# Kernel tuning notes

Measured on AMD Instinct MI355X. Metric: run time of the kernel, lower is better.

## Reference

```python
import jax, jax.numpy as jnp
import numpy as np

N_CLUSTERS = 10

def _conv(x, w, b, stride):
    y = jax.lax.conv_general_dilated(x, w, stride, 'VALID', dimension_numbers=('NCHW', 'OIHW', 'NCHW'))
    return y + b[None, :, None, None]

def _forward(x, conv1_w, conv1_b, conv2_w, conv2_b, conv3_w, conv3_b,
             anc0_w, anc0_b, anc1_w, anc1_b, anc2_w, anc2_b, anc3_w, anc3_b,
             W1_w, W1_b, U_w, U_b, V_w, V_b, Wa_w, Wa_b,
             cluster_w, cluster_b, cls_w, cls_b):
    # backbone: three stride-2 valid convs
    h1 = _conv(x, conv1_w, conv1_b, (2, 2))
    h2 = _conv(h1, conv2_w, conv2_b, (2, 2))
    h3 = _conv(h2, conv3_w, conv3_b, (2, 2))  # [1,512,63,63]
    ancs = [_conv(h3, anc0_w, anc0_b, (1, 1)),
            _conv(h3, anc1_w, anc1_b, (1, 1)),
            _conv(h3, anc2_w, anc2_b, (1, 1)),
            _conv(h3, anc3_w, anc3_b, (1, 1))]
    ksizes = [(3, 3), (1, 1), (3, 1), (1, 3)]
    Hf, Wf = h3.shape[2], h3.shape[3]
    feats, coords = [], []
    # feat_organizer: flatten each anchor map to [Ha*Wa, 1024] and build normalized box coords
    for a, (kh, kw) in zip(ancs, ksizes):
        C, Ha, Wa = a.shape[1], a.shape[2], a.shape[3]
        feats.append(a[0].reshape(C, Ha * Wa).T)
        ys, xs = jnp.meshgrid(jnp.arange(Ha, dtype=jnp.float32), jnp.arange(Wa, dtype=jnp.float32), indexing='ij')
        cx = (xs.reshape(-1) + kw * 0.5) / Wf
        cy = (ys.reshape(-1) + kh * 0.5) / Hf
        bw = jnp.full((Ha * Wa,), kw / Wf, jnp.float32)
        bh = jnp.full((Ha * Wa,), kh / Hf, jnp.float32)
        coords.append(jnp.stack([cx, cy, bw, bh], axis=1))
    feat = jnp.concatenate(feats, 0)      # [N,1024]
    coords = jnp.concatenate(coords, 0)   # [N,4]
    # gated-attention MLP (AttentionHead)
    hmid = jax.nn.relu(feat @ W1_w.T + W1_b)              # [N,512]
    u = jax.nn.sigmoid(hmid @ U_w.T + U_b)                # [N,256]
    v = jnp.tanh(hmid @ V_w.T + V_b)                      # [N,256]
    att = jax.nn.sigmoid((u * v) @ Wa_w.T + Wa_b)[:, 0]   # [N]
    # cluster_features: rank anchors by attention, split into equal clusters,
    # attention-weighted segment reduce of features and box coords per cluster
    N = att.shape[0]
    rank = jnp.argsort(jnp.argsort(-att))
    cid = (rank * N_CLUSTERS) // N                         # [N] int cluster ids
    sw = jax.ops.segment_sum(att, cid, num_segments=N_CLUSTERS)                       # [nc]
    fc = jax.ops.segment_sum(hmid * att[:, None], cid, num_segments=N_CLUSTERS) / (sw[:, None] + 1e-8)   # [nc,512]
    pc = jax.ops.segment_sum(coords * att[:, None], cid, num_segments=N_CLUSTERS) / (sw[:, None] + 1e-8) # [nc,4]
    # ClusterAttention: conv with kernel (1,512) == per-cluster dot product, softmax over clusters
    scores = fc @ cluster_w + cluster_b                    # [nc]
    att_c = jax.nn.softmax(scores)
    # attention_pooling: attention-weighted sum of cluster features
    final = (att_c[:, None] * fc).sum(0, keepdims=True)    # [1,512]
    logits = final @ cls_w.T + cls_b
    return jax.nn.softmax(logits, axis=1), att_c.reshape(1, N_CLUSTERS, 1), pc

def setup_inputs() -> dict:
    key = jax.random.key(0)
    ks = jax.random.split(key, 30)
    def rn(k, shape, scale=0.02):
        return jax.random.normal(k, shape, jnp.float32) * scale
    d = {}
    d['x'] = jax.random.normal(ks[0], (1, 3, 512, 512), jnp.float32)
    d['conv1_w'] = rn(ks[1], (128, 3, 3, 3));    d['conv1_b'] = jnp.zeros((128,), jnp.float32)
    d['conv2_w'] = rn(ks[2], (256, 128, 3, 3));  d['conv2_b'] = jnp.zeros((256,), jnp.float32)
    d['conv3_w'] = rn(ks[3], (512, 256, 3, 3));  d['conv3_b'] = jnp.zeros((512,), jnp.float32)
    d['anc0_w'] = rn(ks[4], (1024, 512, 3, 3));  d['anc0_b'] = jnp.zeros((1024,), jnp.float32)
    d['anc1_w'] = rn(ks[5], (1024, 512, 1, 1));  d['anc1_b'] = jnp.zeros((1024,), jnp.float32)
    d['anc2_w'] = rn(ks[6], (1024, 512, 3, 1));  d['anc2_b'] = jnp.zeros((1024,), jnp.float32)
    d['anc3_w'] = rn(ks[7], (1024, 512, 1, 3));  d['anc3_b'] = jnp.zeros((1024,), jnp.float32)
    d['W1_w'] = rn(ks[8], (512, 1024));          d['W1_b'] = jnp.zeros((512,), jnp.float32)
    d['U_w'] = rn(ks[9], (256, 512));            d['U_b'] = jnp.zeros((256,), jnp.float32)
    d['V_w'] = rn(ks[10], (256, 512));           d['V_b'] = jnp.zeros((256,), jnp.float32)
    d['Wa_w'] = rn(ks[11], (1, 256));            d['Wa_b'] = jnp.zeros((1,), jnp.float32)
    d['cluster_w'] = rn(ks[12], (512,));         d['cluster_b'] = jnp.zeros((), jnp.float32)
    d['cls_w'] = rn(ks[13], (10, 512));          d['cls_b'] = jnp.zeros((10,), jnp.float32)
    return d

def reference(x, conv1_w, conv1_b, conv2_w, conv2_b, conv3_w, conv3_b,
              anc0_w, anc0_b, anc1_w, anc1_b, anc2_w, anc2_b, anc3_w, anc3_b,
              W1_w, W1_b, U_w, U_b, V_w, V_b, Wa_w, Wa_b,
              cluster_w, cluster_b, cls_w, cls_b):
    return _forward(x, conv1_w, conv1_b, conv2_w, conv2_b, conv3_w, conv3_b,
                    anc0_w, anc0_b, anc1_w, anc1_b, anc2_w, anc2_b, anc3_w, anc3_b,
                    W1_w, W1_b, U_w, U_b, V_w, V_b, Wa_w, Wa_b,
                    cluster_w, cluster_b, cls_w, cls_b)
```

## Files before the change

### kernel.cpp

```cpp
#include <hip/hip_runtime.h>
#include <math.h>


#define NTOT 15376
#define PHALF 2032128
typedef unsigned short u16;
typedef unsigned long long u64;
typedef __attribute__((ext_vector_type(8))) short bf16x8;
typedef __attribute__((ext_vector_type(4))) float f32x4;

static __device__ __forceinline__ u16 f2bf(float x) {
    union { float f; unsigned u; } v; v.f = x;
    unsigned r = v.u + 0x7FFF + ((v.u >> 16) & 1);
    return (u16)(r >> 16);
}
static __device__ __forceinline__ float bf2f(u16 h) {
    union { unsigned u; float f; } v; v.u = ((unsigned)h) << 16;
    return v.f;
}

static __device__ __forceinline__ void glds16(const void* g, void* l) {
    __builtin_amdgcn_global_load_lds(
        (const __attribute__((address_space(1))) void*)g,
        (__attribute__((address_space(3))) void*)l,
        16, 0, 0);
}

__global__ __launch_bounds__(256) void prep_all(
    const float* __restrict__ s4, const float* __restrict__ s5,
    const float* __restrict__ s6, const float* __restrict__ s7,
    const float* __restrict__ s8, u16* __restrict__ Wpk,
    u16* __restrict__ UVsep,
    const float* __restrict__ c1w, u16* __restrict__ Wc1pk,
    const float* __restrict__ x, u16* __restrict__ x_t,
    const float* __restrict__ W1w, const float* __restrict__ W1b,
    const float* __restrict__ b0, const float* __restrict__ b1,
    const float* __restrict__ b2, const float* __restrict__ b3,
    float* __restrict__ hb)
{
    int b = blockIdx.x, t = threadIdx.x;
    if (b < 8832) {
        long i = (long)b * 256 + t;
        if (i >= 2260992L) return;
        if (i < 524288L) {
            Wpk[8388608L + i] = f2bf(s4[i]);
        } else if (i < 786432L) {
            long loc = i - 524288L;
            int ic = (int)(loc % 512);
            long row = loc / 512;
            const float* src = (row & 1) ? s6 : s5;
            UVsep[loc] = f2bf(src[(row >> 1) * 512 + ic]);
        } else if (i < 1081344L) {
            long loc = i - 786432L;
            int ic = (int)(loc % 128);
            long r = loc / 128;
            int tt = (int)(r % 9);
            long oc = r / 9;
            Wpk[9175040L + loc] = f2bf(s7[(oc * 128 + ic) * 9 + tt]);
        } else {
            long loc = i - 1081344L;
            int ic = (int)(loc % 256);
            long r = loc / 256;
            int tt = (int)(r % 9);
            long oc = r / 9;
            Wpk[9469952L + loc] = f2bf(s8[(oc * 256 + ic) * 9 + tt]);
        }
    } else if (b < 8864) {
        int j = (b - 8832) * 256 + t;
        if (j < 8192) {
            int oc = j >> 6, k = j & 63;
            Wc1pk[j] = (k < 27) ? f2bf(c1w[oc * 27 + k]) : (u16)0;
        }
    } else if (b < 9119) {
        int sp = (b - 8864) * 256 + t;
        if (sp < 65025) {
            int oy = sp / 255, ox = sp - oy * 255;
            const float* base = x + (long)oy * 2 * 512 + ox * 2;
            u64 pk[16];
#pragma unroll
            for (int q = 0; q < 16; ++q) pk[q] = 0;
#pragma unroll
            for (int ic = 0; ic < 3; ++ic)
#pragma unroll
                for (int ky = 0; ky < 3; ++ky)
#pragma unroll
                    for (int kx = 0; kx < 3; ++kx) {
                        int k = ic * 9 + ky * 3 + kx;
                        float v = base[ic * 262144 + ky * 512 + kx];
                        pk[k >> 2] |= (u64)f2bf(v) << ((k & 3) * 16);
                    }
            u64* drow = (u64*)(x_t + (long)sp * 64);
#pragma unroll
            for (int q = 0; q < 16; ++q) drow[q] = pk[q];
        }
    } else {
        int w = t >> 6, l = t & 63;
        int idx = (b - 9119) * 4 + w;
        int a = idx >> 9, m = idx & 511;
        const float* ab = (a == 0) ? b0 : (a == 1) ? b1 : (a == 2) ? b2 : b3;
        float s = 0.f;
        for (int j = l; j < 1024; j += 64)
            s = fmaf(W1w[(long)m * 1024 + j], ab[j], s);
#pragma unroll
        for (int d = 1; d < 64; d <<= 1) s += __shfl_xor(s, d, 64);
        if (l == 0) hb[idx] = s + W1b[m];
    }
}

__global__ __launch_bounds__(256) void packT_anchor(
    const float* __restrict__ a0w, const float* __restrict__ a1w,
    const float* __restrict__ a2w, const float* __restrict__ a3w,
    u16* __restrict__ WpkT)
{
    __shared__ u16 tile[64][65];
    int bid = blockIdx.x;
    int ocb = bid & 15;
    int rt  = bid >> 4;
    const float* src; int kbase, NT;
    if      (rt < 72)  { src = a0w; kbase = 0;    NT = 9; }
    else if (rt < 80)  { src = a1w; kbase = 4608; NT = 1; }
    else if (rt < 104) { src = a2w; kbase = 5120; NT = 3; }
    else               { src = a3w; kbase = 6656; NT = 3; }
    int kloc0 = rt * 64 - kbase;
    int tap = kloc0 >> 9, ic0 = kloc0 & 511;
    int t = threadIdx.x, q = t >> 6, ln = t & 63;
#pragma unroll
    for (int i = 0; i < 16; ++i) {
        int ocl = q * 16 + i;
        tile[ocl][ln] = f2bf(src[((long)(ocb * 64 + ocl) * 512 + ic0 + ln) * NT + tap]);
    }
    __syncthreads();
#pragma unroll
    for (int i = 0; i < 16; ++i) {
        int kl = q * 16 + i;
        WpkT[(long)(rt * 64 + kl) * 1024 + ocb * 64 + ln] = tile[ln][kl];
    }
}

__global__ __launch_bounds__(256) void combA(
    const float* __restrict__ P, const float* __restrict__ hb,
    u16* __restrict__ Hfeat)
{
    int row = blockIdx.x;
    int oy = row / 61, ox = row - oy * 61;
    long n = (long)(oy * 63 + ox) * 512;
    int c = threadIdx.x * 2;
    float2 p0 = *(const float2*)(P + n + c);
    float2 p1 = *(const float2*)(P + PHALF + n + c);
    float2 bv = *(const float2*)(hb + c);
    float sx = (p0.x + p1.x) + bv.x;
    float sy = (p0.y + p1.y) + bv.y;
    unsigned pk = (unsigned)f2bf(fmaxf(sx, 0.f))
                | ((unsigned)f2bf(fmaxf(sy, 0.f)) << 16);
    *(unsigned*)(Hfeat + (long)row * 512 + c) = pk;
}

__global__ __launch_bounds__(256) void comb3(
    const float* __restrict__ P, const float* __restrict__ bias,
    u16* __restrict__ h3T)
{
    int row = blockIdx.x;
    int trg = (row / 63) * 65 + row % 63;
    long n = (long)row * 512;
    int c = threadIdx.x * 2;
    float2 q0 = *(const float2*)(P + n + c);
    float2 q1 = *(const float2*)(P + PHALF + n + c);
    float2 b  = *(const float2*)(bias + c);
    unsigned pk = (unsigned)f2bf(q0.x + q1.x + b.x)
                | ((unsigned)f2bf(q0.y + q1.y + b.y) << 16);
    *(unsigned*)(h3T + (long)trg * 512 + c) = pk;
}

template<int CMODE, int EMODE, int TMODE>
__global__ __launch_bounds__(256) void gemm_bt(
    const u16* __restrict__ A, const u16* __restrict__ B,
    const float* __restrict__ bias0, const float* __restrict__ bias1,
    const float* __restrict__ bias2, const float* __restrict__ bias3,
    void* __restrict__ Cout, float* __restrict__ Pbuf,
    int M, int N, int RSB, int Ktot, int OH, int OW, int obase)
{
    __shared__ u16 As[4096];
    __shared__ u16 Bs[8192];
    const int tid = threadIdx.x, w = tid >> 6, l = tid & 63;
    const int wr = w >> 1, wc = w & 1;
    const int sl = l & 7, sh = l >> 3, sx = sl ^ sh;

    int n0, m0;
    bool TW3 = false;
    int part = -1;
    int tbase = 0;
    const float* bias = bias0;
    constexpr int ICL2 = (TMODE == 5) ? 1 : (TMODE == 6) ? 2 : (TMODE == 9) ? 0 : 3;
    constexpr int ICK  = 1 << ICL2;
    int ntaps;

    if (TMODE == 8) {
        int job = blockIdx.x >> 8, sub = blockIdx.x & 255;
        n0 = (sub & 31) * 128; m0 = (sub >> 5) * 64;
        int anc;
        if      (job == 0) { anc = 0; ntaps = 4; tbase = 0; part = 0; }
        else if (job == 1) { anc = 0; ntaps = 5; tbase = 4; part = 1; }
        else if (job == 2) { anc = 1; ntaps = 1; }
        else if (job == 3) { anc = 2; ntaps = 3; }
        else               { anc = 3; ntaps = 3; }
        TW3 = (anc == 0 || anc == 3);
        A += (anc == 0) ? 0 : (anc == 1) ? 4608 : (anc == 2) ? 5120 : 6656;
        obase = (anc == 0) ? 0 : (anc == 1) ? 3721 : (anc == 2) ? 7690 : 11533;
        OH = (anc == 0 || anc == 2) ? 61 : 63;
        OW = (anc == 0 || anc == 3) ? 61 : 63;
        bias = bias0 + anc * 512;
    } else if (TMODE == 6 && EMODE == 7) {
        int half = blockIdx.y >> 3;
        n0 = blockIdx.x * 128; m0 = (blockIdx.y & 7) * 64;
        ntaps = half ? 5 : 4; tbase = half * 4;
        Cout = (void*)((float*)Cout + (long)half * PHALF);
    } else {
        n0 = blockIdx.x * 128; m0 = blockIdx.y * 64;
        ntaps = Ktot >> ICL2;
    }
    const long RSA = (TMODE == 8) ? 8192 : (long)Ktot * 64;
    const long RSB2 = (long)RSB * 2;

    int offB[4], ldsOffB[4], ldsOffA[2];
    const char* aBase[2];
    const char* bBase[4];
#pragma unroll
    for (int j = 0; j < 4; ++j) {
        int r = w * 32 + j * 8 + sh;
        int gn = n0 + r;
        if (CMODE == 0)      { gn = min(gn, 3968);  offB[j] = (gn / 63) * 65 + (gn % 63); }
        else if (CMODE == 1) { offB[j] = min(gn, N - 1); }
        else if (CMODE == 2) { gn = min(gn, 16128); offB[j] = (gn / 127) * 510 + (gn % 127) * 2; }
        else                 { gn = min(gn, 3968);  offB[j] = (gn / 63) * 254 + (gn % 63) * 2; }
        ldsOffB[j] = r * 128;
        bBase[j] = (const char*)B + (long)offB[j] * RSB2 + sx * 16;
    }
#pragma unroll
    for (int j = 0; j < 2; ++j) {
        int r = w * 16 + j * 8 + sh;
        ldsOffA[j] = r * 128;
        aBase[j] = (const char*)A + (long)(m0 + r) * RSA * 2 + sx * 16;
    }

    f32x4 acc[2][4];
#pragma unroll
    for (int a = 0; a < 2; ++a)
#pragma unroll
        for (int b = 0; b < 4; ++b) acc[a][b] = (f32x4){0.f, 0.f, 0.f, 0.f};

    for (int t_ = 0; t_ < ntaps; ++t_) {
        int te = t_ + tbase;
        long tOffB;
        if (TMODE == 8) {
            int trow_;
            if (TW3) { int q_ = (te * 11) >> 5; trow_ = q_ * 65 + (te - q_ * 3); }
            else       trow_ = te * 65;
            tOffB = (long)trow_ * RSB2;
        } else if (TMODE == 4) {
            tOffB = (long)te * 1024;
        } else if (TMODE == 5) {
            int q_ = (te * 11) >> 5;
            tOffB = (long)(q_ * 255 + (te - q_ * 3)) * RSB2;
        } else if (TMODE == 6) {
            int q_ = (te * 11) >> 5;
            tOffB = (long)(q_ * 127 + (te - q_ * 3)) * RSB2;
        } else {
            tOffB = 0;
        }
        long aOff = (long)te * (ICK * 128);
#pragma unroll
        for (int kb = 0; kb < ICK; ++kb) {
#pragma unroll
            for (int j = 0; j < 2; ++j)
                glds16(aBase[j] + aOff + kb * 128, (char*)As + ldsOffA[j]);
#pragma unroll
            for (int j = 0; j < 4; ++j)
                glds16(bBase[j] + tOffB + kb * 128, (char*)Bs + ldsOffB[j]);
            __syncthreads();
#pragma unroll
            for (int kk = 0; kk < 2; ++kk) {
                bf16x8 af[2], bfr[4];
#pragma unroll
                for (int f = 0; f < 2; ++f) {
                    int rm = wr * 32 + f * 16 + (l & 15);
                    af[f] = *(const bf16x8*)((const char*)As + rm * 128 +
                               (((kk * 4 + (l >> 4)) ^ (rm & 7)) * 16));
                }
#pragma unroll
                for (int f = 0; f < 4; ++f) {
                    int rn = wc * 64 + f * 16 + (l & 15);
                    bfr[f] = *(const bf16x8*)((const char*)Bs + rn * 128 +
                               (((kk * 4 + (l >> 4)) ^ (rn & 7)) * 16));
                }
#pragma unroll
                for (int fm = 0; fm < 2; ++fm)
#pragma unroll
                    for (int fn = 0; fn < 4; ++fn)
                        acc[fm][fn] = __builtin_amdgcn_mfma_f32_16x16x32_bf16(
                            af[fm], bfr[fn], acc[fm][fn], 0, 0, 0);
            }
            __syncthreads();
        }
    }

#pragma unroll
    for (int fm = 0; fm < 2; ++fm) {
        int gmb = m0 + wr * 32 + fm * 16 + (l >> 4) * 4;
#pragma unroll
        for (int fn = 0; fn < 4; ++fn) {
            int gn = n0 + wc * 64 + fn * 16 + (l & 15);
            f32x4 v = acc[fm][fn];
            if (EMODE == 2) {
                if (gn < N) {
                    int j0 = gmb >> 1;
                    float u0 = 1.f / (1.f + expf(-(v.x + bias0[j0])));
                    float t0 = tanhf(v.y + bias1[j0]);
                    float u1 = 1.f / (1.f + expf(-(v.z + bias0[j0 + 1])));
                    float t1 = tanhf(v.w + bias1[j0 + 1]);
                    float2 o = { u0 * t0 * bias2[j0], u1 * t1 * bias2[j0 + 1] };
                    *(float2*)((float*)Cout + (long)gn * 256 + j0) = o;
                }
            } else if (EMODE == 4) {
                if (gn < N) {
                    float4 bv = *(const float4*)(bias + gmb);
                    u64 pk = (u64)f2bf(v.x + bv.x)
                           | ((u64)f2bf(v.y + bv.y) << 16)
                           | ((u64)f2bf(v.z + bv.z) << 32)
                           | ((u64)f2bf(v.w + bv.w) << 48);
                    *(u64*)((u16*)Cout + (long)gn * M + gmb) = pk;
                }
            } else if (EMODE == 5) {
                if (TMODE == 8 && part >= 0) {
                    if (gn < 3969) {
                        float4 o = { v.x, v.y, v.z, v.w };
                        *(float4*)(Pbuf + (long)part * PHALF + (long)gn * 512 + gmb) = o;
                    }
                } else if (gn < 3969) {
                    int oy = gn / 63, ox = gn - oy * 63;
                    if (oy < OH && ox < OW) {
                        int trg = obase + oy * OW + ox;
                        float4 bv = *(const float4*)(bias + gmb);
                        u64 pk = (u64)f2bf(fmaxf(v.x + bv.x, 0.f))
                               | ((u64)f2bf(fmaxf(v.y + bv.y, 0.f)) << 16)
                               | ((u64)f2bf(fmaxf(v.z + bv.z, 0.f)) << 32)
                               | ((u64)f2bf(fmaxf(v.w + bv.w, 0.f)) << 48);
                        *(u64*)((u16*)Cout + (long)trg * M + gmb) = pk;
                    }
                }
            } else if (EMODE == 6) {
                if (gn < N) {
                    u64 pk = (u64)f2bf(v.x)
                           | ((u64)f2bf(v.y) << 16)
                           | ((u64)f2bf(v.z) << 32)
                           | ((u64)f2bf(v.w) << 48);
                    *(u64*)((u16*)Cout + (long)gn * M + gmb) = pk;
                }
            } else {
                if (gn < 3969) {
                    float4 o = { v.x, v.y, v.z, v.w };
                    *(float4*)((float*)Cout + (long)gn * 512 + gmb) = o;
                }
            }
        }
    }
}

__global__ __launch_bounds__(256) void att_v3(
    const float* __restrict__ UVw, const float* __restrict__ Wab,
    float* __restrict__ att, int* __restrict__ rank, int N)
{
    int t = threadIdx.x, l = t & 63, r = t >> 6;
    int n = blockIdx.x * 4 + r;
    if (t < 4 && blockIdx.x * 4 + t < N) rank[blockIdx.x * 4 + t] = 0;
    if (n >= N) return;
    float4 p = *(const float4*)(UVw + (long)n * 256 + l * 4);
    float s = (p.x + p.y) + (p.z + p.w);
#pragma unroll
    for (int d = 1; d < 64; d <<= 1) s += __shfl_xor(s, d, 64);
    if (l == 0) att[n] = 1.f / (1.f + expf(-(s + Wab[0])));
}

__global__ __launch_bounds__(256) void rank_partial(
    const float* __restrict__ att, int* __restrict__ rank, int N)
{
    __shared__ float sa[1024];
    int n = blockIdx.x * 256 + threadIdx.x;
    int base = blockIdx.y * 1024;
    int cnt = min(1024, N - base);
    for (int t = threadIdx.x; t < cnt; t += 256) sa[t] = att[base + t];
    __syncthreads();
    if (n >= N) return;
    float a = att[n];
    int r = 0;
    for (int t = 0; t < cnt; ++t) {
        float aj = sa[t];
        int j = base + t;
        r += (int)(aj > a) | ((int)(aj == a) & (int)(j < n));
    }
    atomicAdd(&rank[n], r);
}

#define FC_NB 256
#define FC_ROWS 61
__device__ __forceinline__ void anchor_coords(int n, float& cx, float& cy,
                                              float& bw, float& bh)
{
    int kh, kw, Wa, loc;
    if (n < 3721)       { kh = 3; kw = 3; Wa = 61; loc = n; }
    else if (n < 7690)  { kh = 1; kw = 1; Wa = 63; loc = n - 3721; }
    else if (n < 11533) { kh = 3; kw = 1; Wa = 63; loc = n - 7690; }
    else                { kh = 1; kw = 3; Wa = 61; loc = n - 11533; }
    int iy = loc / Wa, ix = loc - iy * Wa;
    cx = (ix + kw * 0.5f) * (1.f / 63.f);
    cy = (iy + kh * 0.5f) * (1.f / 63.f);
    bw = kw * (1.f / 63.f);
    bh = kh * (1.f / 63.f);
}

__global__ __launch_bounds__(256) void tail_part(
    const u16* __restrict__ Hfeat, const float* __restrict__ att,
    const int* __restrict__ rank, float* __restrict__ fcp,
    float* __restrict__ prt, int N)
{
    __shared__ float red[4][50];
    int t = threadIdx.x;
    if (blockIdx.x < FC_NB) {
        int b = blockIdx.x;
        int l = t & 63, r = t >> 6;
        float acc[10][8];
#pragma unroll
        for (int k = 0; k < 10; ++k)
#pragma unroll
            for (int e = 0; e < 8; ++e) acc[k][e] = 0.f;
        int n0 = b * FC_ROWS;
        for (int it = 0; it < 16; ++it) {
            int nl = it * 4 + r;
            int n = n0 + nl;
            if (nl >= FC_ROWS || n >= N) break;
            float a = att[n];
            int c = (rank[n] * 10) / N;
            bf16x8 h8 = *(const bf16x8*)(Hfeat + (long)n * 512 + l * 8);
            float hf[8];
#pragma unroll
            for (int e = 0; e < 8; ++e) hf[e] = bf2f((u16)h8[e]);
#pragma unroll
            for (int k = 0; k < 10; ++k) {
                float sel = (c == k) ? a : 0.f;
#pragma unroll
                for (int e = 0; e < 8; ++e)
                    acc[k][e] = fmaf(sel, hf[e], acc[k][e]);
            }
        }
        float* dst = fcp + (long)b * 5120 + l * 8;
#pragma unroll
        for (int k = 0; k < 10; ++k)
#pragma unroll
            for (int e = 0; e < 8; ++e) dst[k * 512 + e] = acc[k][e];
    } else {
        int b = blockIdx.x - FC_NB;
        int n = b * 256 + t;
        int l = t & 63, w = t >> 6;
        float a = 0.f, cx = 0.f, cy = 0.f, bw = 0.f, bh = 0.f;
        int c = -1;
        if (n < N) {
            a = att[n]; c = (rank[n] * 10) / N;
            anchor_coords(n, cx, cy, bw, bh);
        }
#pragma unroll
        for (int k = 0; k < 10; ++k) {
            float sel = (c == k) ? a : 0.f;
            float v[5] = {sel, sel * cx, sel * cy, sel * bw, sel * bh};
#pragma unroll
            for (int d = 0; d < 5; ++d) {
                float x = v[d];
#pragma unroll
                for (int s = 1; s < 64; s <<= 1) x += __shfl_xor(x, s, 64);
                if (l == 0) red[w][k * 5 + d] = x;
            }
        }
        __syncthreads();
        if (t < 50) prt[b * 50 + t] = red[0][t] + red[1][t] + red[2][t] + red[3][t];
    }
}

__global__ __launch_bounds__(256) void fc_sum(
    const float* __restrict__ fcp, float* __restrict__ fc_raw)
{
    int i = blockIdx.x * 256 + threadIdx.x;
    if (i >= 5120) return;
    float s = 0.f;
    for (int b = 0; b < FC_NB; ++b) s += fcp[(long)b * 5120 + i];
    fc_raw[i] = s;
}

__global__ __launch_bounds__(512) void final_kernel(
    const float* __restrict__ fc_raw, const float* __restrict__ prt,
    const float* __restrict__ cluster_w, const float* __restrict__ cluster_b,
    const float* __restrict__ cls_w, const float* __restrict__ cls_b,
    float* __restrict__ out)
{
    __shared__ float red[512];
    __shared__ float swpc[50];
    int t = threadIdx.x;
    if (t < 50) {
        float s = 0.f;
        for (int b = 0; b < 61; ++b) s += prt[b * 50 + t];
        swpc[t] = s;
    }
    __syncthreads();
    float fcn[10];
#pragma unroll
    for (int k = 0; k < 10; ++k)
        fcn[k] = fc_raw[k * 512 + t] / (swpc[k * 5] + 1e-8f);
    float cw = cluster_w[t];
    float sc[10];
#pragma unroll
    for (int k = 0; k < 10; ++k) {
        red[t] = fcn[k] * cw;
        __syncthreads();
        for (int s = 256; s > 0; s >>= 1) {
            if (t < s) red[t] += red[t + s];
            __syncthreads();
        }
        sc[k] = red[0] + cluster_b[0];
        __syncthreads();
    }
    float mx = sc[0];
#pragma unroll
    for (int k = 1; k < 10; ++k) mx = fmaxf(mx, sc[k]);
    float se = 0.f;
#pragma unroll
    for (int k = 0; k < 10; ++k) { sc[k] = expf(sc[k] - mx); se += sc[k]; }
    float inv = 1.f / se;
#pragma unroll
    for (int k = 0; k < 10; ++k) sc[k] *= inv;
    float fm = 0.f;
#pragma unroll
    for (int k = 0; k < 10; ++k) fm = fmaf(sc[k], fcn[k], fm);
    float lg[10];
#pragma unroll
    for (int c = 0; c < 10; ++c) {
        red[t] = fm * cls_w[c * 512 + t];
        __syncthreads();
        for (int s = 256; s > 0; s >>= 1) {
            if (t < s) red[t] += red[t + s];
            __syncthreads();
        }
        lg[c] = red[0] + cls_b[c];
        __syncthreads();
    }
    float mx2 = lg[0];
#pragma unroll
    for (int c = 1; c < 10; ++c) mx2 = fmaxf(mx2, lg[c]);
    float se2 = 0.f;
#pragma unroll
    for (int c = 0; c < 10; ++c) { lg[c] = expf(lg[c] - mx2); se2 += lg[c]; }
    float inv2 = 1.f / se2;
    if (t < 10) out[t] = lg[t] * inv2;
    if (t >= 10 && t < 20) out[t] = sc[t - 10];
    if (t >= 20 && t < 60) {
        int i = t - 20;
        int k = i >> 2, d = i & 3;
        out[t] = swpc[k * 5 + 1 + d] / (swpc[k * 5] + 1e-8f);
    }
}

extern "C" void kernel_launch(void* const* d_in, const int* in_sizes, int n_in,
                              void* d_out, int out_size, void* d_ws, size_t ws_size,
                              hipStream_t stream)
{
    const float* x    = (const float*)d_in[0];
    const float* c1w  = (const float*)d_in[1];   const float* c1b = (const float*)d_in[2];
    const float* c2w  = (const float*)d_in[3];   const float* c2b = (const float*)d_in[4];
    const float* c3w  = (const float*)d_in[5];   const float* c3b = (const float*)d_in[6];
    const float* a0w  = (const float*)d_in[7];   const float* a0b = (const float*)d_in[8];
    const float* a1w  = (const float*)d_in[9];   const float* a1b = (const float*)d_in[10];
    const float* a2w  = (const float*)d_in[11];  const float* a2b = (const float*)d_in[12];
    const float* a3w  = (const float*)d_in[13];  const float* a3b = (const float*)d_in[14];
    const float* W1w  = (const float*)d_in[15];  const float* W1b = (const float*)d_in[16];
    const float* Uw   = (const float*)d_in[17];  const float* Ub  = (const float*)d_in[18];
    const float* Vw   = (const float*)d_in[19];  const float* Vb  = (const float*)d_in[20];
    const float* Waw  = (const float*)d_in[21];  const float* Wab = (const float*)d_in[22];
    const float* clw  = (const float*)d_in[23];  const float* clb = (const float*)d_in[24];
    const float* clsw = (const float*)d_in[25];  const float* clsb= (const float*)d_in[26];
    float* out = (float*)d_out;

    float* ws = (float*)d_ws;
    u16*   Hfeat= (u16*)ws;
    u16*   h1T  = (u16*)(ws + 3936256);
    u16*   h2T  = (u16*)(ws + 8097856);
    u16*   h3T  = (u16*)(ws + 10162368);
    float* UVw  = ws + 11243968;
    u16*   x_t  = (u16*)(ws + 11243968);
    u16*   Wpk  = (u16*)(ws + 15180224);
    float* P    = ws + 15180224;
    u16*   WpkT = (u16*)(ws + 20505024);
    u16*   WcAll= (u16*)(ws + 24699328);
    float* hb   = ws + 26796480;
    float* att  = ws + 26798528;
    int*   rank = (int*)(ws + 26813904);
    float* fcr  = ws + 26829280;
    float* fcp  = ws + 26834400;
    float* prt  = ws + 28145120;
    u16*   Wc1pk= (u16*)(ws + 28148224);
    u16*   UVpk = (u16*)(ws + 28152320);

    u16* W1pk  = Wpk + 8388608;
    u16* Wc2pk = Wpk + 9175040;
    u16* Wc3pk = Wpk + 9469952;

    dim3 blk(256);
    const float* nul = nullptr;
    float* fnul = nullptr;

    packT_anchor<<<dim3(2048), blk, 0, stream>>>(a0w, a1w, a2w, a3w, WpkT);
    prep_all<<<dim3(9631), blk, 0, stream>>>(W1w, Uw, Vw, c2w, c3w, Wpk, UVpk,
                                             c1w, Wc1pk, x, x_t, W1w, W1b,
                                             a0b, a1b, a2b, a3b, hb);

    gemm_bt<1,4,9><<<dim3(509, 2), blk, 0, stream>>>(Wc1pk, x_t, c1b, nul, nul, nul, h1T, fnul, 128, 65025, 64, 1, 0, 0, 0);

    gemm_bt<1,6,4><<<dim3(4, 128), blk, 0, stream>>>(WpkT, W1pk, nul, nul, nul, nul, WcAll, fnul, 8192, 512, 1024, 16, 0, 0, 0);

    gemm_bt<2,4,5><<<dim3(127, 4), blk, 0, stream>>>(Wc2pk, h1T, c2b, nul, nul, nul, h2T, fnul, 256, 16129, 128, 18, 0, 0, 0);
    gemm_bt<3,7,6><<<dim3(32, 16), blk, 0, stream>>>(Wc3pk, h2T, nul, nul, nul, nul, P, fnul, 512, 3969, 256, 36, 0, 0, 0);
    comb3<<<dim3(3969), blk, 0, stream>>>(P, c3b, h3T);

    gemm_bt<0,5,8><<<dim3(1280), blk, 0, stream>>>(WcAll, h3T, hb, nul, nul, nul, Hfeat, P, 512, 3969, 512, 0, 0, 0, 0);
    combA<<<dim3(3721), blk, 0, stream>>>(P, hb, Hfeat);

    gemm_bt<1,2,1><<<dim3(121, 8), blk, 0, stream>>>(UVpk, Hfeat, Ub, Vb, Waw, nul, UVw, fnul, 512, NTOT, 512, 8, 0, 0, 0);

    att_v3<<<dim3(3844), blk, 0, stream>>>(UVw, Wab, att, rank, NTOT);
    rank_partial<<<dim3(61, 16), blk, 0, stream>>>(att, rank, NTOT);
    tail_part<<<dim3(FC_NB + 61), blk, 0, stream>>>(Hfeat, att, rank, fcp, prt, NTOT);
    fc_sum<<<dim3(20), blk, 0, stream>>>(fcp, fcr);
    final_kernel<<<dim3(1), dim3(512), 0, stream>>>(fcr, prt, clw, clb, clsw, clsb, out);
}
```

Before: 284.4 us.

## Fuse small launches and rebalance anchor-0 split-K into three parts

Folds the anchor weight transpose-pack into the prep_all kernel as extra blocks, and merges the conv1 GEMM with the combined-weight GEMM into one launch through a shared device-side gemm body. This cuts kernel launches and lets independent work run together. It also splits the 9-tap anchor-0 GEMM into three 3-tap partial jobs instead of 4+5, with combA summing a third partial buffer, to balance block work. The extra partial adds P-buffer traffic and assumes the workspace has room for a third PHALF slice.

```diff
diff --git a/kernel.cpp b/kernel.cpp
--- a/kernel.cpp
+++ b/kernel.cpp
@@ -36,8 +36,12 @@
     const float* __restrict__ W1w, const float* __restrict__ W1b,
     const float* __restrict__ b0, const float* __restrict__ b1,
     const float* __restrict__ b2, const float* __restrict__ b3,
-    float* __restrict__ hb)
-{
+    float* __restrict__ hb,
+    const float* __restrict__ a0w, const float* __restrict__ a1w,
+    const float* __restrict__ a2w, const float* __restrict__ a3w,
+    u16* __restrict__ WpkT)
+{
+    __shared__ u16 tile[64][65];
     int b = blockIdx.x, t = threadIdx.x;
     if (b < 8832) {
         long i = (long)b * 256 + t;
@@ -93,7 +97,7 @@
 #pragma unroll
             for (int q = 0; q < 16; ++q) drow[q] = pk[q];
         }
-    } else {
+    } else if (b < 9631) {
         int w = t >> 6, l = t & 63;
         int idx = (b - 9119) * 4 + w;
         int a = idx >> 9, m = idx & 511;
@@ -104,36 +108,29 @@
 #pragma unroll
         for (int d = 1; d < 64; d <<= 1) s += __shfl_xor(s, d, 64);
         if (l == 0) hb[idx] = s + W1b[m];
-    }
-}
-
-__global__ __launch_bounds__(256) void packT_anchor(
-    const float* __restrict__ a0w, const float* __restrict__ a1w,
-    const float* __restrict__ a2w, const float* __restrict__ a3w,
-    u16* __restrict__ WpkT)
-{
-    __shared__ u16 tile[64][65];
-    int bid = blockIdx.x;
-    int ocb = bid & 15;
-    int rt  = bid >> 4;
-    const float* src; int kbase, NT;
-    if      (rt < 72)  { src = a0w; kbase = 0;    NT = 9; }
-    else if (rt < 80)  { src = a1w; kbase = 4608; NT = 1; }
-    else if (rt < 104) { src = a2w; kbase = 5120; NT = 3; }
-    else               { src = a3w; kbase = 6656; NT = 3; }
-    int kloc0 = rt * 64 - kbase;
-    int tap = kloc0 >> 9, ic0 = kloc0 & 511;
-    int t = threadIdx.x, q = t >> 6, ln = t & 63;
-#pragma unroll
-    for (int i = 0; i < 16; ++i) {
-        int ocl = q * 16 + i;
-        tile[ocl][ln] = f2bf(src[((long)(ocb * 64 + ocl) * 512 + ic0 + ln) * NT + tap]);
-    }
-    __syncthreads();
-#pragma unroll
-    for (int i = 0; i < 16; ++i) {
-        int kl = q * 16 + i;
-        WpkT[(long)(rt * 64 + kl) * 1024 + ocb * 64 + ln] = tile[ln][kl];
+    } else {
+        int bid = b - 9631;
+        int ocb = bid & 15;
+        int rt  = bid >> 4;
+        const float* src; int kbase, NT;
+        if      (rt < 72)  { src = a0w; kbase = 0;    NT = 9; }
+        else if (rt < 80)  { src = a1w; kbase = 4608; NT = 1; }
+        else if (rt < 104) { src = a2w; kbase = 5120; NT = 3; }
+        else               { src = a3w; kbase = 6656; NT = 3; }
+        int kloc0 = rt * 64 - kbase;
+        int tap = kloc0 >> 9, ic0 = kloc0 & 511;
+        int q = t >> 6, ln = t & 63;
+#pragma unroll
+        for (int i = 0; i < 16; ++i) {
+            int ocl = q * 16 + i;
+            tile[ocl][ln] = f2bf(src[((long)(ocb * 64 + ocl) * 512 + ic0 + ln) * NT + tap]);
+        }
+        __syncthreads();
+#pragma unroll
+        for (int i = 0; i < 16; ++i) {
+            int kl = q * 16 + i;
+            WpkT[(long)(rt * 64 + kl) * 1024 + ocb * 64 + ln] = tile[ln][kl];
+        }
     }
 }
 
@@ -147,9 +144,10 @@
     int c = threadIdx.x * 2;
     float2 p0 = *(const float2*)(P + n + c);
     float2 p1 = *(const float2*)(P + PHALF + n + c);
+    float2 p2 = *(const float2*)(P + 2L * PHALF + n + c);
     float2 bv = *(const float2*)(hb + c);
-    float sx = (p0.x + p1.x) + bv.x;
-    float sy = (p0.y + p1.y) + bv.y;
+    float sx = (p0.x + p1.x) + p2.x + bv.x;
+    float sy = (p0.y + p1.y) + p2.y + bv.y;
     unsigned pk = (unsigned)f2bf(fmaxf(sx, 0.f))
                 | ((unsigned)f2bf(fmaxf(sy, 0.f)) << 16);
     *(unsigned*)(Hfeat + (long)row * 512 + c) = pk;
@@ -172,15 +170,14 @@
 }
 
 template<int CMODE, int EMODE, int TMODE>
-__global__ __launch_bounds__(256) void gemm_bt(
+static __device__ __forceinline__ void gemm_body(
+    int bx, int by, u16* As, u16* Bs,
     const u16* __restrict__ A, const u16* __restrict__ B,
     const float* __restrict__ bias0, const float* __restrict__ bias1,
     const float* __restrict__ bias2, const float* __restrict__ bias3,
     void* __restrict__ Cout, float* __restrict__ Pbuf,
     int M, int N, int RSB, int Ktot, int OH, int OW, int obase)
 {
-    __shared__ u16 As[4096];
-    __shared__ u16 Bs[8192];
     const int tid = threadIdx.x, w = tid >> 6, l = tid & 63;
     const int wr = w >> 1, wc = w & 1;
     const int sl = l & 7, sh = l >> 3, sx = sl ^ sh;
@@ -195,13 +192,14 @@
     int ntaps;
 
     if (TMODE == 8) {
-        int job = blockIdx.x >> 8, sub = blockIdx.x & 255;
+        int job = bx >> 8, sub = bx & 255;
         n0 = (sub & 31) * 128; m0 = (sub >> 5) * 64;
         int anc;
-        if      (job == 0) { anc = 0; ntaps = 4; tbase = 0; part = 0; }
-        else if (job == 1) { anc = 0; ntaps = 5; tbase = 4; part = 1; }
-        else if (job == 2) { anc = 1; ntaps = 1; }
-        else if (job == 3) { anc = 2; ntaps = 3; }
+        if      (job == 0) { anc = 0; ntaps = 3; tbase = 0; part = 0; }
+        else if (job == 1) { anc = 0; ntaps = 3; tbase = 3; part = 1; }
+        else if (job == 2) { anc = 0; ntaps = 3; tbase = 6; part = 2; }
+        else if (job == 3) { anc = 1; ntaps = 1; }
+        else if (job == 4) { anc = 2; ntaps = 3; }
         else               { anc = 3; ntaps = 3; }
         TW3 = (anc == 0 || anc == 3);
         A += (anc == 0) ? 0 : (anc == 1) ? 4608 : (anc == 2) ? 5120 : 6656;
@@ -210,12 +208,12 @@
         OW = (anc == 0 || anc == 3) ? 61 : 63;
         bias = bias0 + anc * 512;
     } else if (TMODE == 6 && EMODE == 7) {
-        int half = blockIdx.y >> 3;
-        n0 = blockIdx.x * 128; m0 = (blockIdx.y & 7) * 64;
+        int half = by >> 3;
+        n0 = bx * 128; m0 = (by & 7) * 64;
         ntaps = half ? 5 : 4; tbase = half * 4;
         Cout = (void*)((float*)Cout + (long)half * PHALF);
     } else {
-        n0 = blockIdx.x * 128; m0 = blockIdx.y * 64;
+        n0 = bx * 128; m0 = by * 64;
         ntaps = Ktot >> ICL2;
     }
     const long RSA = (TMODE == 8) ? 8192 : (long)Ktot * 64;
@@ -365,6 +363,42 @@
     }
 }
 
+template<int CMODE, int EMODE, int TMODE>
+__global__ __launch_bounds__(256) void gemm_k(
+    const u16* __restrict__ A, const u16* __restrict__ B,
+    const float* __restrict__ bias0, const float* __restrict__ bias1,
+    const float* __restrict__ bias2, const float* __restrict__ bias3,
+    void* __restrict__ Cout, float* __restrict__ Pbuf,
+    int M, int N, int RSB, int Ktot, int OH, int OW, int obase)
+{
+    __shared__ u16 As[4096];
+    __shared__ u16 Bs[8192];
+    gemm_body<CMODE, EMODE, TMODE>(blockIdx.x, blockIdx.y, As, Bs, A, B,
+                                   bias0, bias1, bias2, bias3, Cout, Pbuf,
+                                   M, N, RSB, Ktot, OH, OW, obase);
+}
+
+__global__ __launch_bounds__(256) void conv1_wc_k(
+    const u16* __restrict__ Wc1pk, const u16* __restrict__ x_t,
+    const float* __restrict__ c1b, u16* __restrict__ h1T,
+    const u16* __restrict__ WpkT, const u16* __restrict__ W1pk,
+    u16* __restrict__ WcAll)
+{
+    __shared__ u16 As[4096];
+    __shared__ u16 Bs[8192];
+    int bid = blockIdx.x;
+    if (bid < 1018) {
+        gemm_body<1, 4, 9>(bid % 509, bid / 509, As, Bs, Wc1pk, x_t,
+                           c1b, nullptr, nullptr, nullptr, h1T, nullptr,
+                           128, 65025, 64, 1, 0, 0, 0);
+    } else {
+        int b2 = bid - 1018;
+        gemm_body<1, 6, 4>(b2 & 3, b2 >> 2, As, Bs, WpkT, W1pk,
+                           nullptr, nullptr, nullptr, nullptr, WcAll, nullptr,
+                           8192, 512, 1024, 16, 0, 0, 0);
+    }
+}
+
 __global__ __launch_bounds__(256) void att_v3(
     const float* __restrict__ UVw, const float* __restrict__ Wab,
     float* __restrict__ att, int* __restrict__ rank, int N)
@@ -613,23 +647,22 @@
     const float* nul = nullptr;
     float* fnul = nullptr;
 
-    packT_anchor<<<dim3(2048), blk, 0, stream>>>(a0w, a1w, a2w, a3w, WpkT);
-    prep_all<<<dim3(9631), blk, 0, stream>>>(W1w, Uw, Vw, c2w, c3w, Wpk, UVpk,
-                                             c1w, Wc1pk, x, x_t, W1w, W1b,
-                                             a0b, a1b, a2b, a3b, hb);
-
-    gemm_bt<1,4,9><<<dim3(509, 2), blk, 0, stream>>>(Wc1pk, x_t, c1b, nul, nul, nul, h1T, fnul, 128, 65025, 64, 1, 0, 0, 0);
-
-    gemm_bt<1,6,4><<<dim3(4, 128), blk, 0, stream>>>(WpkT, W1pk, nul, nul, nul, nul, WcAll, fnul, 8192, 512, 1024, 16, 0, 0, 0);
-
-    gemm_bt<2,4,5><<<dim3(127, 4), blk, 0, stream>>>(Wc2pk, h1T, c2b, nul, nul, nul, h2T, fnul, 256, 16129, 128, 18, 0, 0, 0);
-    gemm_bt<3,7,6><<<dim3(32, 16), blk, 0, stream>>>(Wc3pk, h2T, nul, nul, nul, nul, P, fnul, 512, 3969, 256, 36, 0, 0, 0);
+    prep_all<<<dim3(11679), blk, 0, stream>>>(W1w, Uw, Vw, c2w, c3w, Wpk, UVpk,
+                                              c1w, Wc1pk, x, x_t, W1w, W1b,
+                                              a0b, a1b, a2b, a3b, hb,
+                                              a0w, a1w, a2w, a3w, WpkT);
+
+    conv1_wc_k<<<dim3(1530), blk, 0, stream>>>(Wc1pk, x_t, c1b, h1T,
+                                               WpkT, W1pk, WcAll);
+
+    gemm_k<2,4,5><<<dim3(127, 4), blk, 0, stream>>>(Wc2pk, h1T, c2b, nul, nul, nul, h2T, fnul, 256, 16129, 128, 18, 0, 0, 0);
+    gemm_k<3,7,6><<<dim3(32, 16), blk, 0, stream>>>(Wc3pk, h2T, nul, nul, nul, nul, P, fnul, 512, 3969, 256, 36, 0, 0, 0);
     comb3<<<dim3(3969), blk, 0, stream>>>(P, c3b, h3T);
 
-    gemm_bt<0,5,8><<<dim3(1280), blk, 0, stream>>>(WcAll, h3T, hb, nul, nul, nul, Hfeat, P, 512, 3969, 512, 0, 0, 0, 0);
+    gemm_k<0,5,8><<<dim3(1536), blk, 0, stream>>>(WcAll, h3T, hb, nul, nul, nul, Hfeat, P, 512, 3969, 512, 0, 0, 0, 0);
     combA<<<dim3(3721), blk, 0, stream>>>(P, hb, Hfeat);
 
-    gemm_bt<1,2,1><<<dim3(121, 8), blk, 0, stream>>>(UVpk, Hfeat, Ub, Vb, Waw, nul, UVw, fnul, 512, NTOT, 512, 8, 0, 0, 0);
+    gemm_k<1,2,1><<<dim3(121, 8), blk, 0, stream>>>(UVpk, Hfeat, Ub, Vb, Waw, nul, UVw, fnul, 512, NTOT, 512, 8, 0, 0, 0);
 
     att_v3<<<dim3(3844), blk, 0, stream>>>(UVw, Wab, att, rank, NTOT);
     rank_partial<<<dim3(61, 16), blk, 0, stream>>>(att, rank, NTOT);
```

Result: no change. 282.9 us (-0.5%).
